# Kernel optimization log

Hardware: AMD Instinct MI355X
Metric: run time of the kernel (lower is better)

## Reference

```python
import jax, jax.numpy as jnp
from jax import lax
import numpy as np

B, N, C = 4, 2000, 80           # images, proposals/img, foreground classes
SCORE_THR = 0.05
IOU_THR = 0.5
MAX_PER_IMG = 100
K_PRE = 2000                     # pre-NMS top-k candidates per image
STDS = np.array([0.1, 0.1, 0.2, 0.2], dtype=np.float32)
MAX_RATIO = float(abs(np.log(16.0 / 1000.0)))  # wh_ratio_clip=16/1000


def setup_inputs() -> dict:
    key = jax.random.key(0)
    k1, k2, k3 = jax.random.split(key, 3)
    class_outs = jax.random.normal(k1, (B, N, C + 1), dtype=jnp.float32)
    regression_outs = jax.random.normal(k2, (B, N, C * 4), dtype=jnp.float32) * 0.5
    # random valid proposal boxes inside 800x1333 images (x1<x2, y1<y2)
    xy = jax.random.uniform(k3, (B, N, 2, 2), dtype=jnp.float32)
    xy = xy * jnp.array([1333.0, 800.0], dtype=jnp.float32)
    lo = jnp.min(xy, axis=2)
    hi = jnp.max(xy, axis=2) + 1.0
    boxes = jnp.concatenate([lo, hi], axis=-1)  # [B,N,4] x1,y1,x2,y2
    images_hw = jnp.tile(jnp.array([[800, 1333]], dtype=jnp.int32), (B, 1))
    return {"class_outs": class_outs, "regression_outs": regression_outs,
            "boxes": boxes, "images_hw": images_hw}


def _decode(props, deltas, h, w):
    # props [N,4], deltas [N,C,4] -> decoded boxes [N,C,4], clipped to image
    d = deltas * jnp.asarray(STDS)
    dx, dy, dw, dh = d[..., 0], d[..., 1], d[..., 2], d[..., 3]
    dw = jnp.clip(dw, -MAX_RATIO, MAX_RATIO)
    dh = jnp.clip(dh, -MAX_RATIO, MAX_RATIO)
    px = (props[:, None, 0] + props[:, None, 2]) * 0.5
    py = (props[:, None, 1] + props[:, None, 3]) * 0.5
    pw = props[:, None, 2] - props[:, None, 0]
    ph = props[:, None, 3] - props[:, None, 1]
    gx = px + pw * dx
    gy = py + ph * dy
    gw = pw * jnp.exp(dw)
    gh = ph * jnp.exp(dh)
    x1 = jnp.clip(gx - gw * 0.5, 0.0, w)
    y1 = jnp.clip(gy - gh * 0.5, 0.0, h)
    x2 = jnp.clip(gx + gw * 0.5, 0.0, w)
    y2 = jnp.clip(gy + gh * 0.5, 0.0, h)
    return jnp.stack([x1, y1, x2, y2], axis=-1)


def _pairwise_iou(b):
    # b [K,4] -> iou [K,K]
    area = (b[:, 2] - b[:, 0]) * (b[:, 3] - b[:, 1])
    lt = jnp.maximum(b[:, None, :2], b[None, :, :2])
    rb = jnp.minimum(b[:, None, 2:], b[None, :, 2:])
    wh = jnp.clip(rb - lt, 0.0)
    inter = wh[..., 0] * wh[..., 1]
    return inter / (area[:, None] + area[None, :] - inter + 1e-6)


def _process_image(cls_out, reg_out, props, hw):
    h = hw[0].astype(jnp.float32)
    w = hw[1].astype(jnp.float32)
    scores = jax.nn.softmax(cls_out, axis=-1)[:, :C]          # drop background col
    bboxes = _decode(props, reg_out.reshape(N, C, 4), h, w)   # [N,C,4]
    flat_scores = scores.reshape(-1)                          # [N*C]
    flat_boxes = bboxes.reshape(-1, 4)
    labels = jnp.tile(jnp.arange(C, dtype=jnp.int32), N)      # class fastest-varying
    cand = jnp.where(flat_scores > SCORE_THR, flat_scores, -1.0)
    top_scores, top_idx = lax.top_k(cand, K_PRE)
    top_boxes = flat_boxes[top_idx]
    top_labels = labels[top_idx]
    valid = top_scores > SCORE_THR
    # class-offset trick: boxes of distinct classes never overlap
    off = top_labels.astype(jnp.float32)[:, None] * (jnp.maximum(h, w) + 1.0)
    iou = _pairwise_iou(top_boxes + off)                      # [K_PRE,K_PRE]
    idxs = jnp.arange(K_PRE)

    def body(i, keep):
        sup = (idxs > i) & (iou[i] > IOU_THR) & keep[i]
        return keep & ~sup

    keep = lax.fori_loop(0, K_PRE, body, valid)
    kept_scores = jnp.where(keep, top_scores, -1.0)
    det_scores, det_i = lax.top_k(kept_scores, MAX_PER_IMG)
    det_valid = det_scores > SCORE_THR
    det_boxes = jnp.where(det_valid[:, None], top_boxes[det_i], 0.0)
    det_labels = jnp.where(det_valid, top_labels[det_i], -1)
    det_scores = jnp.where(det_valid, det_scores, 0.0)
    return det_boxes, det_scores, det_labels


def reference(class_outs, regression_outs, boxes, images_hw):
    det_boxes, det_scores, det_labels = jax.vmap(_process_image)(
        class_outs, regression_outs, boxes, images_hw)
    return det_boxes, det_scores, det_labels
```

## Files before the change

kernel.cpp:

```cpp
#include <hip/hip_runtime.h>


typedef unsigned long long u64;
typedef unsigned int u32;

#define B_ 4
#define N_ 2000
#define C_ 80
#define NCLS 81
#define KPRE 2000
#define MAXDET 100
#define TARGET 400
#define NB 2312
#define NBPAD 2368
#define NG 37
#define HBASE 0xF500
#define KSHIFT 46
#define CAPA 512
#define CAPB 2048
#define NWAVE 16
#define SEGW 384
#define CAPBLK 128
#define BPI 125
#define BIGI 0x7fffffff

__device__ __forceinline__ u64 pack_key(float score, unsigned fi) {
  return ((u64)__float_as_uint(score) << 32) | (u64)(0xFFFFFFFFu - fi);
}

__device__ __forceinline__ int dpp_min8(int v) {
  int t;
  t = __builtin_amdgcn_update_dpp(BIGI, v, 0x104, 0xF, 0xF, false);
  v = min(v, t);
  t = __builtin_amdgcn_update_dpp(BIGI, v, 0x102, 0xF, 0xF, false);
  v = min(v, t);
  t = __builtin_amdgcn_update_dpp(BIGI, v, 0x101, 0xF, 0xF, false);
  v = min(v, t);
  return v;
}

__device__ __forceinline__ float4 decode_one(
    u64 kk, const float* __restrict__ reg, const float* __restrict__ props,
    int b, float h, float w, float offscale) {
  const float MAXR = 4.135166556742356f;
  unsigned fi = 0xFFFFFFFFu - (u32)kk;
  int n = (int)(fi / (unsigned)C_);
  int c = (int)(fi - (unsigned)n * (unsigned)C_);
  float4 p = ((const float4*)props)[b * N_ + n];
  const float* dl = reg + ((size_t)(b * N_ + n)) * (C_ * 4) + c * 4;
  float dx = dl[0] * 0.1f;
  float dy = dl[1] * 0.1f;
  float dw = fminf(fmaxf(dl[2] * 0.2f, -MAXR), MAXR);
  float dh = fminf(fmaxf(dl[3] * 0.2f, -MAXR), MAXR);
  float px = (p.x + p.z) * 0.5f, py = (p.y + p.w) * 0.5f;
  float pw = p.z - p.x, ph = p.w - p.y;
  float gx = px + pw * dx, gy = py + ph * dy;
  float gw = pw * expf(dw), gh = ph * expf(dh);
  float off = (float)c * offscale;
  return make_float4(fminf(fmaxf(gx - gw * 0.5f, 0.0f), w) + off,
                     fminf(fmaxf(gy - gh * 0.5f, 0.0f), h) + off,
                     fminf(fmaxf(gx + gw * 0.5f, 0.0f), w) + off,
                     fminf(fmaxf(gy + gh * 0.5f, 0.0f), h) + off);
}

__global__ __launch_bounds__(1024) void cand_kernel(
    const float* __restrict__ cls, u64* __restrict__ gkeys, int* __restrict__ gcnt) {
  __shared__ int s_wc[16], s_woff[16];
  const int tid = threadIdx.x;
  const int w = tid >> 6, lane = tid & 63;
  const int blk = blockIdx.x;
  const int b = blk / BPI;
  const int n = (blk % BPI) * 16 + w;
  const float* lg = cls + (size_t)(b * N_ + n) * NCLS;
  float x0 = lg[lane];
  float x1 = (lane < 17) ? lg[64 + lane] : -3.0e38f;
  float mx = fmaxf(x0, x1);
#pragma unroll
  for (int o = 32; o > 0; o >>= 1) mx = fmaxf(mx, __shfl_xor(mx, o));
  float e0 = expf(x0 - mx);
  float e1 = (lane < 17) ? expf(x1 - mx) : 0.0f;
  float sum = e0 + e1;
#pragma unroll
  for (int o = 32; o > 0; o >>= 1) sum += __shfl_xor(sum, o);
  float sc0 = e0 / sum, sc1 = e1 / sum;
  bool p0 = sc0 > 0.05f;
  bool p1 = (lane < 16) && (sc1 > 0.05f);
  u64 m0 = __ballot(p0), m1 = __ballot(p1);
  int c0 = __popcll(m0);
  if (lane == 0) s_wc[w] = c0 + __popcll(m1);
  __syncthreads();
  if (tid == 0) {
    int acc = 0;
#pragma unroll
    for (int i = 0; i < 16; ++i) { s_woff[i] = acc; acc += s_wc[i]; }
    gcnt[blk] = acc;
  }
  __syncthreads();
  const int base = s_woff[w];
  const u64 lt = (1ull << lane) - 1;
  u64* gk = gkeys + (size_t)blk * CAPBLK;
  if (p0) {
    int slot = base + __popcll(m0 & lt);
    if (slot < CAPBLK) gk[slot] = pack_key(sc0, (unsigned)(n * C_ + lane));
  }
  if (p1) {
    int slot = base + c0 + __popcll(m1 & lt);
    if (slot < CAPBLK) gk[slot] = pack_key(sc1, (unsigned)(n * C_ + 64 + lane));
  }
}


__global__ __launch_bounds__(1024) void nms_kernel(
    const float* __restrict__ reg, const float* __restrict__ props,
    const int* __restrict__ hw, const u64* __restrict__ gkeys,
    const int* __restrict__ gcnt, float* __restrict__ out) {
  __shared__ u64 lds8[7952];
  char* bp = (char*)lds8;
  u64* keylist = (u64*)bp;
  u64* SS = (u64*)bp;
  u64* rb = (u64*)(bp + 8192);
  u64* U2 = (u64*)bp;
  u64* SSB = (u64*)(bp + 16384);
  u32* hist = (u32*)(bp + 49152);
  float4* bxA = (float4*)(bp + 49152);
  u64* U = (u64*)(bp + 58624);
  int* outl = (int*)(bp + 62720);
  int* misc = (int*)(bp + 63232);
  int* segc = (int*)(bp + 63296);
  int* s_coarse = (int*)(bp + 63360);

  const int b = blockIdx.x, tid = threadIdx.x;
  const int wv = tid >> 6, lane = tid & 63;

  float h = (float)hw[b * 2 + 0];
  float w = (float)hw[b * 2 + 1];
  float offscale = fmaxf(h, w) + 1.0f;

  if (tid < 16) misc[tid] = 0;
  if (tid < 64) s_coarse[tid] = 0;
  for (int i = tid; i < NBPAD; i += 1024) hist[i] = 0;
  __syncthreads();

  {
    int cnts[8];
#pragma unroll
    for (int k = 0; k < 8; k++) {
      int p = wv + 16 * k;
      cnts[k] = (p < BPI) ? gcnt[b * BPI + p] : 0;
    }
    bool ovf = false;
    int segoff = 0;
#pragma unroll
    for (int k = 0; k < 8; k++) {
      int p = wv + 16 * k;
      if (p >= BPI) break;
      int cnt = cnts[k];
      if (cnt > CAPBLK) { ovf = true; cnt = CAPBLK; }
      const u64* seg = gkeys + (size_t)(b * BPI + p) * CAPBLK;
#pragma unroll
      for (int r = 0; r < 2; r++) {
        int idx = lane + 64 * r;
        if (idx < cnt) {
          u64 key = seg[idx];
          int bi = min(max((int)(key >> KSHIFT) - HBASE, 0), NB - 1);
          atomicAdd(&hist[bi], 1u);
          int slot = segoff + idx;
          if (slot < SEGW) keylist[wv * SEGW + slot] = key;
        }
      }
      segoff += cnt;
    }
    if (segoff > SEGW) ovf = true;
    if (lane == 0) {
      segc[wv] = min(segoff, SEGW);
      if (ovf) misc[7] = 1;
    }
  }
  __syncthreads();

  for (int g2 = wv; g2 < NG; g2 += NWAVE) {
    int v = (int)hist[(g2 << 6) | lane];
#pragma unroll
    for (int o = 32; o; o >>= 1) v += __shfl_xor(v, o);
    if (lane == 0) s_coarse[g2] = v;
  }
  __syncthreads();

  if (tid < 64) {
    int v = s_coarse[lane];
#pragma unroll
    for (int off = 1; off < 64; off <<= 1) {
      int src = lane + off;
      int o = __shfl(v, src < 64 ? src : 63);
      if (src < 64) v += o;
    }
    int Mtot = __shfl(v, 0);
    u64 pm = __ballot(v >= TARGET);
    int T_A = 0, S_A;
    if (pm) {
      int gs = 63 - __builtin_clzll(pm);
      int beyond = __shfl(v, gs + 1);
      int fv = (int)hist[(gs << 6) | lane];
#pragma unroll
      for (int off = 1; off < 64; off <<= 1) {
        int src = lane + off;
        int o = __shfl(fv, src < 64 ? src : 63);
        if (src < 64) fv += o;
      }
      int cum = beyond + fv;
      u64 pm2 = __ballot(cum >= TARGET);
      int tr = 63 - __builtin_clzll(pm2);
      T_A = (gs << 6) + tr;
      S_A = __shfl(cum, tr);
    } else {
      S_A = Mtot;
    }
    u64 pmB = __ballot(v >= KPRE);
    int T_B = 0, S_B;
    if (pmB) {
      int gs = 63 - __builtin_clzll(pmB);
      int beyond = __shfl(v, gs + 1);
      int fv = (int)hist[(gs << 6) | lane];
#pragma unroll
      for (int off = 1; off < 64; off <<= 1) {
        int src = lane + off;
        int o = __shfl(fv, src < 64 ? src : 63);
        if (src < 64) fv += o;
      }
      int cum = beyond + fv;
      u64 pm2 = __ballot(cum >= KPRE);
      int tr = 63 - __builtin_clzll(pm2);
      T_B = (gs << 6) + tr;
      S_B = __shfl(cum, tr);
    } else {
      S_B = Mtot;
    }
    if (lane == 0) {
      misc[0] = T_A; misc[2] = S_A; misc[3] = Mtot;
      misc[1] = T_B; misc[8] = S_B; misc[4] = 0;
    }
  }
  __syncthreads();
  if (tid == 0 && misc[8] > CAPB)
    misc[1] = min(misc[1] + 1, NB - 1);
  __syncthreads();

  int T_A = misc[0], S_A = misc[2], Mtot = misc[3];
  bool modeB = (S_A > CAPA) || (misc[7] != 0);
  int K = 0, nkept = 0;

  if (!modeB) {
    for (int s = 0; s < NWAVE; s++) {
      int Mg = segc[s];
      bool pred = false;
      u64 key = 0;
      if (tid < Mg) {
        key = keylist[s * SEGW + tid];
        int bi = min(max((int)(key >> KSHIFT) - HBASE, 0), NB - 1);
        pred = (bi >= T_A);
      }
      u64 mk = __ballot(pred);
      if (mk) {
        int wbase = 0;
        if (lane == 0) wbase = atomicAdd(&misc[4], __popcll(mk));
        wbase = __shfl(wbase, 0);
        if (pred) {
          int pos = wbase + __popcll(mk & ((1ull << lane) - 1));
          if (pos < CAPA) U[pos] = key;
        }
      }
    }
    __syncthreads();
    int S = misc[4];
    if (S > CAPA) S = CAPA;
    if (tid == 0 && (S & 1)) U[S] = 0ULL;
    __syncthreads();
    if (tid < S) {
      u64 k1 = U[tid];
      int r1 = 0;
      const ulonglong2* Uu2 = (const ulonglong2*)U;
      int half = (S + 1) >> 1;
      for (int k = 0; k < half; k++) {
        ulonglong2 kk = Uu2[k];
        r1 += (kk.x > k1) + (kk.y > k1);
      }
      SS[r1] = k1;
    }
    __syncthreads();
    K = S;
    for (int j = tid; j < K; j += 1024)
      bxA[j] = decode_one(SS[j], reg, props, b, h, w, offscale);
    __syncthreads();

    int nwords = (S + 63) >> 6;
    int ntiles = nwords * (nwords + 1) / 2;
    for (int t = wv; t < ntiles; t += NWAVE) {
      int ti = 0, rem = t;
      while (rem >= nwords - ti) { rem -= nwords - ti; ti++; }
      int tj = ti + rem;
      int i = (ti << 6) + lane;
      float4 bi4 = bxA[i];
      float ai = (bi4.z - bi4.x) * (bi4.w - bi4.y);
      u64 bits = 0;
      int jbase = tj << 6;
      int jcount = min(64, S - jbase);
      for (int jj = 0; jj < jcount; jj++) {
        int j = jbase + jj;
        float4 bj = bxA[j];
        float aj = (bj.z - bj.x) * (bj.w - bj.y);
        float iw = fmaxf(fminf(bi4.z, bj.z) - fmaxf(bi4.x, bj.x), 0.0f);
        float ih = fmaxf(fminf(bi4.w, bj.w) - fmaxf(bi4.y, bj.y), 0.0f);
        float inter = iw * ih;
        float iou = inter / (ai + aj - inter + 1e-6f);
        if (j > i && iou > 0.5f) bits |= (1ull << jj);
      }
      if (i < S) rb[i * 8 + tj] = bits;
    }
    __syncthreads();

    if (tid < 64) {
      u64 alive = 0;
      if (lane < nwords) {
        alive = ~0ull;
        int remb = S & 63;
        if (lane == nwords - 1 && remb) alive = (1ull << remb) - 1;
      }
      int nk = 0;
      if (S > 0) {
        int i = 0;
        for (;;) {
          if (lane == 0) outl[nk] = i;
          nk++;
          if (nk >= MAXDET) break;
          if (lane == (i >> 6)) alive &= ~(1ull << (i & 63));
          u64 row = (lane < nwords) ? rb[i * 8 + lane] : 0ull;
          u64 a2 = alive & ~row;
          alive = a2;
          int cnd = a2 ? ((lane << 6) + (int)__builtin_ctzll(a2)) : BIGI;
          int m8 = dpp_min8(cnd);
          i = __builtin_amdgcn_readfirstlane(m8);
          if (i >= BIGI) break;
        }
      }
      if (lane == 0) misc[6] = nk;
    }
    __syncthreads();
    nkept = misc[6];
    if (nkept < MAXDET && K < Mtot && K < KPRE) modeB = true;
  }

  if (modeB) {
    __syncthreads();
    if (tid == 0) misc[4] = 0;
    __syncthreads();
    int T_B = misc[1];
    for (int k = 0; k < 8; k++) {
      int p = wv + 16 * k;
      if (p >= BPI) break;
      int cnt = min(gcnt[b * BPI + p], CAPBLK);
      const u64* seg = gkeys + (size_t)(b * BPI + p) * CAPBLK;
#pragma unroll
      for (int r = 0; r < 2; r++) {
        int idx = lane + 64 * r;
        bool pred = false;
        u64 key = 0;
        if (idx < cnt) {
          key = seg[idx];
          int bi = min(max((int)(key >> KSHIFT) - HBASE, 0), NB - 1);
          pred = (bi >= T_B);
        }
        u64 mk = __ballot(pred);
        if (mk) {
          int wbase = 0;
          if (lane == 0) wbase = atomicAdd(&misc[4], __popcll(mk));
          wbase = __shfl(wbase, 0);
          if (pred) {
            int pos = wbase + __popcll(mk & ((1ull << lane) - 1));
            if (pos < CAPB) U2[pos] = key;
          }
        }
      }
    }
    __syncthreads();
    int S = misc[4];
    if (S > CAPB) S = CAPB;
    {
      int j1 = tid, j2 = tid + 1024;
      u64 k1 = (j1 < S) ? U2[j1] : 0ULL;
      u64 k2 = (j2 < S) ? U2[j2] : 0ULL;
      int r1 = 0, r2 = 0;
      for (int k = 0; k < S; k++) {
        u64 kk = U2[k];
        r1 += (kk > k1);
        r2 += (kk > k2);
      }
      __syncthreads();
      if (j1 < S) SSB[r1] = k1;
      if (j2 < S) SSB[r2] = k2;
    }
    __syncthreads();
    K = (S < KPRE) ? S : KPRE;
    int j1 = tid, j2 = tid + 1024;
    bool kp1 = (j1 < K), kp2 = (j2 < K);
    float4 bb1 = kp1 ? decode_one(SSB[j1], reg, props, b, h, w, offscale)
                     : make_float4(0, 0, 0, 0);
    float4 bb2 = kp2 ? decode_one(SSB[j2], reg, props, b, h, w, offscale)
                     : make_float4(0, 0, 0, 0);
    int nk = 0;
    if (K > 0) {
      int i = 0;
      for (;;) {
        if (tid == 0) { outl[nk] = i; misc[5] = K; }
        nk++;
        if (nk >= MAXDET) break;
        __syncthreads();
        float4 tb = decode_one(SSB[i], reg, props, b, h, w, offscale);
        float ai = (tb.z - tb.x) * (tb.w - tb.y);
        int ln = K;
        if (kp1 && j1 > i) {
          float aj = (bb1.z - bb1.x) * (bb1.w - bb1.y);
          float iw = fmaxf(fminf(tb.z, bb1.z) - fmaxf(tb.x, bb1.x), 0.0f);
          float ih = fmaxf(fminf(tb.w, bb1.w) - fmaxf(tb.y, bb1.y), 0.0f);
          float inter = iw * ih;
          float iou = inter / (ai + aj - inter + 1e-6f);
          if (iou > 0.5f) kp1 = false;
          else ln = min(ln, j1);
        }
        if (kp2 && j2 > i) {
          float aj = (bb2.z - bb2.x) * (bb2.w - bb2.y);
          float iw = fmaxf(fminf(tb.z, bb2.z) - fmaxf(tb.x, bb2.x), 0.0f);
          float ih = fmaxf(fminf(tb.w, bb2.w) - fmaxf(tb.y, bb2.y), 0.0f);
          float inter = iw * ih;
          float iou = inter / (ai + aj - inter + 1e-6f);
          if (iou > 0.5f) kp2 = false;
          else ln = min(ln, j2);
        }
#pragma unroll
        for (int off = 32; off; off >>= 1) ln = min(ln, __shfl_xor(ln, off));
        if ((tid & 63) == 0 && ln < K) atomicMin(&misc[5], ln);
        __syncthreads();
        int ni = misc[5];
        __syncthreads();
        if (ni >= K) break;
        i = ni;
      }
    }
    if (tid == 0) misc[6] = nk;
    __syncthreads();
    nkept = misc[6];
  }

  float* oBox = out;
  float* oSc = out + B_ * MAXDET * 4;
  float* oLb = out + B_ * MAXDET * 5;
  for (int k2 = tid; k2 < MAXDET; k2 += 1024) {
    float4 bb = make_float4(0.0f, 0.0f, 0.0f, 0.0f);
    float sv = 0.0f, lv = -1.0f;
    if (k2 < nkept) {
      int idx = outl[k2];
      u64 kk = modeB ? SSB[idx] : SS[idx];
      sv = __uint_as_float((u32)(kk >> 32));
      unsigned fi = 0xFFFFFFFFu - (u32)kk;
      int c = (int)(fi % (unsigned)C_);
      float off = (float)c * offscale;
      float4 ob = modeB ? decode_one(kk, reg, props, b, h, w, offscale) : bxA[idx];
      bb = make_float4(ob.x - off, ob.y - off, ob.z - off, ob.w - off);
      lv = (float)c;
    }
    oBox[(b * MAXDET + k2) * 4 + 0] = bb.x;
    oBox[(b * MAXDET + k2) * 4 + 1] = bb.y;
    oBox[(b * MAXDET + k2) * 4 + 2] = bb.z;
    oBox[(b * MAXDET + k2) * 4 + 3] = bb.w;
    oSc[b * MAXDET + k2] = sv;
    oLb[b * MAXDET + k2] = lv;
  }
}

extern "C" void kernel_launch(void* const* d_in, const int* in_sizes, int n_in,
                              void* d_out, int out_size, void* d_ws, size_t ws_size,
                              hipStream_t stream) {
  const float* cls = (const float*)d_in[0];
  const float* reg = (const float*)d_in[1];
  const float* props = (const float*)d_in[2];
  const int* hw = (const int*)d_in[3];
  float* out = (float*)d_out;

  int* gcnt = (int*)d_ws;
  u64* gkeys = (u64*)((char*)d_ws + 2048);

  cand_kernel<<<B_ * BPI, 1024, 0, stream>>>(cls, gkeys, gcnt);
  nms_kernel<<<B_, 1024, 0, stream>>>(reg, props, hw, gkeys, gcnt, out);
}
```

Before: 119.2 us.

## Shrink candidate target, use DPP wave reductions, prefetch next NMS row speculatively

Lowers the mode-A candidate target and capacity so less data is sorted and IoU-tested in the common path. The softmax max and sum reductions switch from shuffle-xor loops to DPP row and broadcast steps plus a readlane. The greedy NMS scan now loads the suppression row for i+1 ahead of time and uses it when the next survivor is i+1, hiding LDS latency in the serial loop. A smaller target raises the risk of falling back to the slower mode B when fewer than 100 boxes survive.

```diff
diff --git a/kernel.cpp b/kernel.cpp
--- a/kernel.cpp
+++ b/kernel.cpp
@@ -10,13 +10,13 @@
 #define NCLS 81
 #define KPRE 2000
 #define MAXDET 100
-#define TARGET 400
+#define TARGET 256
 #define NB 2312
 #define NBPAD 2368
 #define NG 37
 #define HBASE 0xF500
 #define KSHIFT 46
-#define CAPA 512
+#define CAPA 320
 #define CAPB 2048
 #define NWAVE 16
 #define SEGW 384
@@ -26,6 +26,27 @@
 
 __device__ __forceinline__ u64 pack_key(float score, unsigned fi) {
   return ((u64)__float_as_uint(score) << 32) | (u64)(0xFFFFFFFFu - fi);
+}
+
+__device__ __forceinline__ float wred_max(float v) {
+  int t;
+#define STEPM(ctrl)                                                          \
+  t = __builtin_amdgcn_update_dpp(__float_as_int(v), __float_as_int(v),      \
+                                  (ctrl), 0xF, 0xF, false);                  \
+  v = fmaxf(v, __int_as_float(t));
+  STEPM(0x111) STEPM(0x112) STEPM(0x114) STEPM(0x118) STEPM(0x142) STEPM(0x143)
+#undef STEPM
+  return __int_as_float(__builtin_amdgcn_readlane(__float_as_int(v), 63));
+}
+__device__ __forceinline__ float wred_sum(float v) {
+  int t;
+#define STEPS(ctrl)                                                          \
+  t = __builtin_amdgcn_update_dpp(0, __float_as_int(v), (ctrl), 0xF, 0xF,    \
+                                  false);                                    \
+  v = v + __int_as_float(t);
+  STEPS(0x111) STEPS(0x112) STEPS(0x114) STEPS(0x118) STEPS(0x142) STEPS(0x143)
+#undef STEPS
+  return __int_as_float(__builtin_amdgcn_readlane(__float_as_int(v), 63));
 }
 
 __device__ __forceinline__ int dpp_min8(int v) {
@@ -74,14 +95,10 @@
   const float* lg = cls + (size_t)(b * N_ + n) * NCLS;
   float x0 = lg[lane];
   float x1 = (lane < 17) ? lg[64 + lane] : -3.0e38f;
-  float mx = fmaxf(x0, x1);
-#pragma unroll
-  for (int o = 32; o > 0; o >>= 1) mx = fmaxf(mx, __shfl_xor(mx, o));
+  float mx = wred_max(fmaxf(x0, x1));
   float e0 = expf(x0 - mx);
   float e1 = (lane < 17) ? expf(x1 - mx) : 0.0f;
-  float sum = e0 + e1;
-#pragma unroll
-  for (int o = 32; o > 0; o >>= 1) sum += __shfl_xor(sum, o);
+  float sum = wred_sum(e0 + e1);
   float sc0 = e0 / sum, sc1 = e1 / sum;
   bool p0 = sc0 > 0.05f;
   bool p1 = (lane < 16) && (sc1 > 0.05f);
@@ -328,18 +345,22 @@
       int nk = 0;
       if (S > 0) {
         int i = 0;
+        u64 row = (lane < nwords) ? rb[0 * 8 + lane] : 0ull;
         for (;;) {
           if (lane == 0) outl[nk] = i;
           nk++;
           if (nk >= MAXDET) break;
           if (lane == (i >> 6)) alive &= ~(1ull << (i & 63));
-          u64 row = (lane < nwords) ? rb[i * 8 + lane] : 0ull;
+          u64 rowSpec = (i + 1 < S && lane < nwords) ? rb[(i + 1) * 8 + lane] : 0ull;
           u64 a2 = alive & ~row;
           alive = a2;
           int cnd = a2 ? ((lane << 6) + (int)__builtin_ctzll(a2)) : BIGI;
           int m8 = dpp_min8(cnd);
-          i = __builtin_amdgcn_readfirstlane(m8);
-          if (i >= BIGI) break;
+          int ni = __builtin_amdgcn_readfirstlane(m8);
+          if (ni >= BIGI) break;
+          row = (ni == i + 1) ? rowSpec
+                              : ((lane < nwords) ? rb[ni * 8 + lane] : 0ull);
+          i = ni;
         }
       }
       if (lane == 0) misc[6] = nk;
```

Result: faster. 108.0 us (-9.4%).
